# Kernel tuning notes

Measured on AMD Instinct MI355X. Metric: run time of the kernel, lower is better.

Reference implementation:

```python
import jax, jax.numpy as jnp
import numpy as np

E, D, H, K = 8, 768, 3072, 2   # num_experts, embed_size, expert_size, top-k
TAU = 1.0
BN, PN = 32, 196

def l2norm(v):
    # F.normalize(p=2, dim=-1), eps=1e-12
    return v / jnp.maximum(jnp.linalg.norm(v, axis=-1, keepdims=True), 1e-12)

def setup_inputs() -> dict:
    key = jax.random.key(0)
    ks = jax.random.split(key, 8)
    s = 0.02  # weight init scale for stability
    return {
        "x": jax.random.normal(ks[0], (BN, PN, D), dtype=jnp.float32),
        "Wlinear": jax.random.normal(ks[1], (D, D), dtype=jnp.float32) * s,
        "learnedE": jax.random.normal(ks[2], (E, D), dtype=jnp.float32),
        "bias": jnp.zeros((BN * PN, E), dtype=jnp.float32),
        "W1": jax.random.normal(ks[3], (E, D, H), dtype=jnp.float32) * s,
        "b1": jnp.zeros((E, H), dtype=jnp.float32),
        "W2": jax.random.normal(ks[4], (E, H, D), dtype=jnp.float32) * s,
        "b2": jnp.zeros((E, D), dtype=jnp.float32),
        "sW1": jax.random.normal(ks[5], (D, H), dtype=jnp.float32) * s,
        "sb1": jnp.zeros((H,), dtype=jnp.float32),
        "sW2": jax.random.normal(ks[6], (H, D), dtype=jnp.float32) * s,
        "sb2": jnp.zeros((D,), dtype=jnp.float32),
    }

def reference(x, Wlinear, learnedE, bias, W1, b1, W2, b2, sW1, sb1, sW2, sb2):
    bn, pn, d = x.shape
    patches = x.reshape(bn * pn, d)                      # [T, D]
    proj = l2norm(patches @ Wlinear.T)                   # router projection
    routed = proj @ l2norm(learnedE).T                   # [T, E] cosine scores
    probs = jax.nn.softmax((routed + bias) / TAU, axis=1)  # eval path (no noise)
    k_probs, k_idx = jax.lax.top_k(probs, K)             # [T, K]
    # combine weights: scatter top-k probs into dense [T, E] gate matrix
    T = probs.shape[0]
    gates = jnp.zeros_like(probs).at[jnp.arange(T)[:, None], k_idx].add(k_probs)
    # expert MLPs computed densely for all experts, masked by gates
    h = jax.nn.gelu(jnp.einsum('td,edh->teh', patches, W1) + b1[None], approximate=False)
    eo = jnp.einsum('teh,ehd->ted', h, W2) + b2[None]    # [T, E, D]
    moe = jnp.einsum('ted,te->td', eo, gates)            # weighted combine
    # shared expert (expert_list[-1]) applied to every token; dropout is identity in eval
    shared = jax.nn.gelu(patches @ sW1 + sb1, approximate=False) @ sW2 + sb2
    return (moe + shared).reshape(bn, pn, d)
```

## Files before the change

### kernel.cpp

```cpp
#include <hip/hip_runtime.h>
#include <hip/hip_bf16.h>

typedef __hip_bfloat16 bf16;
typedef __attribute__((ext_vector_type(8))) short short8;
typedef __attribute__((ext_vector_type(4))) float f32x4;

#define T_TOK 6272
#define D_DIM 768
#define H_DIM 3072
#define NEXP 8
#define MAXTILES 160

__device__ __forceinline__ void async16(void* lds, const void* g) {
  __builtin_amdgcn_global_load_lds(
      (const __attribute__((address_space(1))) void*)g,
      (__attribute__((address_space(3))) void*)lds, 16, 0, 0);
}


__global__ void cast_hilo(const float* __restrict__ in, bf16* __restrict__ hi,
                          bf16* __restrict__ lo, int n) {
  int i = blockIdx.x * blockDim.x + threadIdx.x;
  int stride = gridDim.x * blockDim.x;
  for (; i < n; i += stride) {
    float x = in[i];
    bf16 h = __float2bfloat16(x);
    hi[i] = h;
    lo[i] = __float2bfloat16(x - __bfloat162float(h));
  }
}

__global__ void transpose_cast(const float* __restrict__ in, bf16* __restrict__ out,
                               int R, int C) {
  __shared__ float tile[32][33];
  int b = blockIdx.z;
  const float* ib = in + (size_t)b * R * C;
  bf16* ob = out + (size_t)b * R * C;
  int r0 = blockIdx.x * 32, c0 = blockIdx.y * 32;
  int tx = threadIdx.x & 31, ty = threadIdx.x >> 5;
  for (int i = 0; i < 32; i += 8)
    tile[ty + i][tx] = ib[(size_t)(r0 + ty + i) * C + c0 + tx];
  __syncthreads();
  for (int i = 0; i < 32; i += 8)
    ob[(size_t)(c0 + ty + i) * R + r0 + tx] = __float2bfloat16(tile[tx][ty + i]);
}

__global__ void norm_learnedE(const float* __restrict__ lE, float* __restrict__ eHat) {
  int wave = threadIdx.x >> 6, lane = threadIdx.x & 63;
  for (int e = wave; e < NEXP; e += 4) {
    float v[12];
    float ss = 0.f;
    for (int j = 0; j < 12; j++) {
      v[j] = lE[e * D_DIM + lane + 64 * j];
      ss += v[j] * v[j];
    }
    for (int o = 32; o; o >>= 1) ss += __shfl_xor(ss, o);
    float rn = 1.f / fmaxf(sqrtf(ss), 1e-12f);
    for (int j = 0; j < 12; j++) eHat[e * D_DIM + lane + 64 * j] = v[j] * rn;
  }
}


__global__ __launch_bounds__(256) void gemm_router(
    const bf16* __restrict__ pHi, const bf16* __restrict__ pLo,
    const bf16* __restrict__ wHi, const bf16* __restrict__ wLo,
    float* __restrict__ y) {
  __shared__ __align__(16) bf16 As[128 * 32];
  __shared__ __align__(16) bf16 Bs[128 * 32];
  int tid = threadIdx.x, wave = tid >> 6, lane = tid & 63;
  int wr = wave >> 1, wc = wave & 1;
  int rowbase = blockIdx.x * 128, colbase = blockIdx.y * 128;
  int sc8 = (lane & 3) * 8;
  f32x4 acc[4][4];
  for (int m = 0; m < 4; m++)
    for (int n = 0; n < 4; n++) acc[m][n] = 0.f;

  for (int ks = 0; ks < 72; ks++) {
    int term = ks / 24;
    int kk = (ks % 24) * 32;
    const bf16* A = (term == 1) ? pLo : pHi;
    const bf16* B = (term == 2) ? wLo : wHi;
    __syncthreads();
    for (int p = 0; p < 2; p++) {
      int r = wave * 32 + p * 16 + (lane >> 2);
      async16(&As[(wave * 32 + p * 16) * 32], A + (size_t)(rowbase + r) * D_DIM + kk + sc8);
      async16(&Bs[(wave * 32 + p * 16) * 32], B + (size_t)(colbase + r) * D_DIM + kk + sc8);
    }
    __syncthreads();
    int koff = (lane >> 4) * 8;
    short8 af[4], bfr[4];
    for (int m = 0; m < 4; m++)
      af[m] = *(const short8*)&As[(wr * 64 + m * 16 + (lane & 15)) * 32 + koff];
    for (int n = 0; n < 4; n++)
      bfr[n] = *(const short8*)&Bs[(wc * 64 + n * 16 + (lane & 15)) * 32 + koff];
    for (int m = 0; m < 4; m++)
      for (int n = 0; n < 4; n++)
        acc[m][n] = __builtin_amdgcn_mfma_f32_16x16x32_bf16(af[m], bfr[n], acc[m][n], 0, 0, 0);
  }
  for (int m = 0; m < 4; m++)
    for (int n = 0; n < 4; n++)
      for (int j = 0; j < 4; j++) {
        int r = rowbase + wr * 64 + m * 16 + (lane >> 4) * 4 + j;
        int c = colbase + wc * 64 + n * 16 + (lane & 15);
        y[(size_t)r * D_DIM + c] = acc[m][n][j];
      }
}


__global__ void router_epi(const float* __restrict__ y, const float* __restrict__ eHat,
                           const float* __restrict__ bias, int* __restrict__ gidx,
                           float* __restrict__ gval, int* __restrict__ counts) {
  int wave = threadIdx.x >> 6, lane = threadIdx.x & 63;
  int t = blockIdx.x * 4 + wave;
  float v[12];
  float ss = 0.f;
  for (int j = 0; j < 12; j++) {
    v[j] = y[(size_t)t * D_DIM + lane + 64 * j];
    ss += v[j] * v[j];
  }
  for (int o = 32; o; o >>= 1) ss += __shfl_xor(ss, o);
  float d[NEXP];
  for (int e = 0; e < NEXP; e++) {
    float s = 0.f;
    for (int j = 0; j < 12; j++) s += v[j] * eHat[e * D_DIM + lane + 64 * j];
    for (int o = 32; o; o >>= 1) s += __shfl_xor(s, o);
    d[e] = s;
  }
  if (lane == 0) {
    float rn = 1.f / fmaxf(sqrtf(ss), 1e-12f);
    float sc[NEXP], mx = -1e30f;
    for (int e = 0; e < NEXP; e++) {
      sc[e] = d[e] * rn + bias[t * NEXP + e];
      mx = fmaxf(mx, sc[e]);
    }
    float p[NEXP], sum = 0.f;
    for (int e = 0; e < NEXP; e++) {
      p[e] = expf(sc[e] - mx);
      sum += p[e];
    }
    float inv = 1.f / sum;
    int i1 = 0;
    for (int e = 1; e < NEXP; e++)
      if (sc[e] > sc[i1]) i1 = e;
    int i2 = -1;
    for (int e = 0; e < NEXP; e++) {
      if (e == i1) continue;
      if (i2 < 0 || sc[e] > sc[i2]) i2 = e;
    }
    gidx[t * 2] = i1;
    gidx[t * 2 + 1] = i2;
    gval[t * 2] = p[i1] * inv;
    gval[t * 2 + 1] = p[i2] * inv;
    atomicAdd(&counts[i1], 1);
    atomicAdd(&counts[i2], 1);
  }
}


__global__ void scan_build(const int* __restrict__ counts, int* __restrict__ segstart,
                           int* __restrict__ cursors, int* __restrict__ tiles,
                           int* __restrict__ numtiles) {
  if (threadIdx.x == 0) {
    int off = 0;
    for (int e = 0; e < NEXP; e++) {
      segstart[e] = off;
      cursors[e] = off;
      off += counts[e];
    }
    segstart[NEXP] = off;
    segstart[NEXP + 1] = off + T_TOK;
    int nt = 0;
    for (int e = 0; e < NEXP + 1; e++) {
      int cnt = (e < NEXP) ? counts[e] : T_TOK;
      int ntl = (cnt + 127) >> 7;
      for (int l = 0; l < ntl; l++) {
        tiles[nt * 2] = e;
        tiles[nt * 2 + 1] = l;
        nt++;
      }
    }
    *numtiles = nt;
  }
}

__global__ void fill_assign(const int* __restrict__ gidx, int* __restrict__ cursors,
                            int* __restrict__ rowtok, int* __restrict__ slot_of) {
  int t = blockIdx.x * 256 + threadIdx.x;
  if (t >= T_TOK) return;
  for (int k = 0; k < 2; k++) {
    int e = gidx[t * 2 + k];
    int pos = atomicAdd(&cursors[e], 1);
    rowtok[pos] = t;
    slot_of[t * 2 + k] = pos;
  }
  rowtok[2 * T_TOK + t] = t;
}


__global__ __launch_bounds__(256) void gemm_ffn1(
    const bf16* __restrict__ pHi, const bf16* __restrict__ W1T,
    const bf16* __restrict__ sW1T, const float* __restrict__ b1,
    const float* __restrict__ sb1, const int* __restrict__ segstart,
    const int* __restrict__ tiles, const int* __restrict__ numtiles,
    const int* __restrict__ rowtok, bf16* __restrict__ hbuf) {
  int gx = blockIdx.x;
  if (gx >= *numtiles) return;
  int seg = tiles[gx * 2], lt = tiles[gx * 2 + 1];
  int s0 = segstart[seg] + lt * 128;
  int send = segstart[seg + 1];
  const bf16* Bw = (seg < NEXP) ? W1T + (size_t)seg * H_DIM * D_DIM : sW1T;
  const float* bb = (seg < NEXP) ? b1 + seg * H_DIM : sb1;

  __shared__ __align__(16) bf16 As[128 * 32];
  __shared__ __align__(16) bf16 Bs[128 * 32];
  int tid = threadIdx.x, wave = tid >> 6, lane = tid & 63;
  int wr = wave >> 1, wc = wave & 1;
  int colbase = blockIdx.y * 128;
  int sc8 = (lane & 3) * 8;

  const bf16* arow[2];
  for (int p = 0; p < 2; p++) {
    int s = s0 + wave * 32 + p * 16 + (lane >> 2);
    if (s > send - 1) s = send - 1;
    arow[p] = pHi + (size_t)rowtok[s] * D_DIM;
  }

  f32x4 acc[4][4];
  for (int m = 0; m < 4; m++)
    for (int n = 0; n < 4; n++) acc[m][n] = 0.f;

  for (int ks = 0; ks < 24; ks++) {
    int kk = ks * 32;
    __syncthreads();
    for (int p = 0; p < 2; p++) {
      int r = wave * 32 + p * 16 + (lane >> 2);
      async16(&As[(wave * 32 + p * 16) * 32], arow[p] + kk + sc8);
      async16(&Bs[(wave * 32 + p * 16) * 32], Bw + (size_t)(colbase + r) * D_DIM + kk + sc8);
    }
    __syncthreads();
    int koff = (lane >> 4) * 8;
    short8 af[4], bfr[4];
    for (int m = 0; m < 4; m++)
      af[m] = *(const short8*)&As[(wr * 64 + m * 16 + (lane & 15)) * 32 + koff];
    for (int n = 0; n < 4; n++)
      bfr[n] = *(const short8*)&Bs[(wc * 64 + n * 16 + (lane & 15)) * 32 + koff];
    for (int m = 0; m < 4; m++)
      for (int n = 0; n < 4; n++)
        acc[m][n] = __builtin_amdgcn_mfma_f32_16x16x32_bf16(af[m], bfr[n], acc[m][n], 0, 0, 0);
  }
  for (int n = 0; n < 4; n++) {
    int c = colbase + wc * 64 + n * 16 + (lane & 15);
    float bv = bb[c];
    for (int m = 0; m < 4; m++)
      for (int j = 0; j < 4; j++) {
        int s = s0 + wr * 64 + m * 16 + (lane >> 4) * 4 + j;
        if (s < send) {
          float xv = acc[m][n][j] + bv;
          float g = 0.5f * xv * (1.f + erff(xv * 0.70710678118654752f));
          hbuf[(size_t)s * H_DIM + c] = __float2bfloat16(g);
        }
      }
  }
}


__global__ __launch_bounds__(256) void gemm_ffn2(
    const bf16* __restrict__ hbuf, const bf16* __restrict__ W2T,
    const bf16* __restrict__ sW2T, const float* __restrict__ b2,
    const float* __restrict__ sb2, const int* __restrict__ segstart,
    const int* __restrict__ tiles, const int* __restrict__ numtiles,
    float* __restrict__ moebuf) {
  int gx = blockIdx.x;
  if (gx >= *numtiles) return;
  int seg = tiles[gx * 2], lt = tiles[gx * 2 + 1];
  int s0 = segstart[seg] + lt * 128;
  int send = segstart[seg + 1];
  const bf16* Bw = (seg < NEXP) ? W2T + (size_t)seg * H_DIM * D_DIM : sW2T;
  const float* bb = (seg < NEXP) ? b2 + seg * D_DIM : sb2;

  __shared__ __align__(16) bf16 As[128 * 32];
  __shared__ __align__(16) bf16 Bs[128 * 32];
  int tid = threadIdx.x, wave = tid >> 6, lane = tid & 63;
  int wr = wave >> 1, wc = wave & 1;
  int colbase = blockIdx.y * 128;
  int sc8 = (lane & 3) * 8;

  f32x4 acc[4][4];
  for (int m = 0; m < 4; m++)
    for (int n = 0; n < 4; n++) acc[m][n] = 0.f;

  for (int ks = 0; ks < 96; ks++) {
    int kk = ks * 32;
    __syncthreads();
    for (int p = 0; p < 2; p++) {
      int r = wave * 32 + p * 16 + (lane >> 2);
      async16(&As[(wave * 32 + p * 16) * 32], hbuf + (size_t)(s0 + r) * H_DIM + kk + sc8);
      async16(&Bs[(wave * 32 + p * 16) * 32], Bw + (size_t)(colbase + r) * H_DIM + kk + sc8);
    }
    __syncthreads();
    int koff = (lane >> 4) * 8;
    short8 af[4], bfr[4];
    for (int m = 0; m < 4; m++)
      af[m] = *(const short8*)&As[(wr * 64 + m * 16 + (lane & 15)) * 32 + koff];
    for (int n = 0; n < 4; n++)
      bfr[n] = *(const short8*)&Bs[(wc * 64 + n * 16 + (lane & 15)) * 32 + koff];
    for (int m = 0; m < 4; m++)
      for (int n = 0; n < 4; n++)
        acc[m][n] = __builtin_amdgcn_mfma_f32_16x16x32_bf16(af[m], bfr[n], acc[m][n], 0, 0, 0);
  }
  for (int n = 0; n < 4; n++) {
    int c = colbase + wc * 64 + n * 16 + (lane & 15);
    float bv = bb[c];
    for (int m = 0; m < 4; m++)
      for (int j = 0; j < 4; j++) {
        int s = s0 + wr * 64 + m * 16 + (lane >> 4) * 4 + j;
        if (s < send) moebuf[(size_t)s * D_DIM + c] = acc[m][n][j] + bv;
      }
  }
}


__global__ void combine_out(const float* __restrict__ moebuf, const float* __restrict__ gval,
                            const int* __restrict__ slot_of, float* __restrict__ out) {
  int i = blockIdx.x * 256 + threadIdx.x;
  const int total = T_TOK * (D_DIM / 4);
  if (i >= total) return;
  int t = i / (D_DIM / 4), c = i % (D_DIM / 4);
  float g0 = gval[2 * t], g1 = gval[2 * t + 1];
  int sA = slot_of[2 * t], sB = slot_of[2 * t + 1];
  const f32x4* pa = (const f32x4*)(moebuf + (size_t)sA * D_DIM) + c;
  const f32x4* pb = (const f32x4*)(moebuf + (size_t)sB * D_DIM) + c;
  const f32x4* ps = (const f32x4*)(moebuf + (size_t)(2 * T_TOK + t) * D_DIM) + c;
  f32x4 r = g0 * (*pa) + g1 * (*pb) + *ps;
  ((f32x4*)out)[i] = r;
}


extern "C" void kernel_launch(void* const* d_in, const int* in_sizes, int n_in,
                              void* d_out, int out_size, void* d_ws, size_t ws_size,
                              hipStream_t stream) {
  const float* x = (const float*)d_in[0];
  const float* Wlinear = (const float*)d_in[1];
  const float* learnedE = (const float*)d_in[2];
  const float* bias = (const float*)d_in[3];
  const float* W1 = (const float*)d_in[4];
  const float* b1 = (const float*)d_in[5];
  const float* W2 = (const float*)d_in[6];
  const float* b2 = (const float*)d_in[7];
  const float* sW1 = (const float*)d_in[8];
  const float* sb1 = (const float*)d_in[9];
  const float* sW2 = (const float*)d_in[10];
  const float* sb2 = (const float*)d_in[11];
  float* out = (float*)d_out;

  char* ws = (char*)d_ws;
  size_t off = 0;
  auto alloc = [&](size_t bytes) {
    char* p = ws + off;
    off += (bytes + 255) & ~(size_t)255;
    return p;
  };
  float* eHat = (float*)alloc(8 * 768 * 4);
  bf16* pHi = (bf16*)alloc((size_t)T_TOK * D_DIM * 2);
  bf16* pLo = (bf16*)alloc((size_t)T_TOK * D_DIM * 2);
  bf16* wHi = (bf16*)alloc((size_t)D_DIM * D_DIM * 2);
  bf16* wLo = (bf16*)alloc((size_t)D_DIM * D_DIM * 2);
  bf16* W1T = (bf16*)alloc((size_t)NEXP * D_DIM * H_DIM * 2);
  bf16* W2T = (bf16*)alloc((size_t)NEXP * D_DIM * H_DIM * 2);
  bf16* sW1T = (bf16*)alloc((size_t)D_DIM * H_DIM * 2);
  bf16* sW2T = (bf16*)alloc((size_t)D_DIM * H_DIM * 2);
  float* y = (float*)alloc((size_t)T_TOK * D_DIM * 4);
  bf16* hbuf = (bf16*)alloc((size_t)3 * T_TOK * H_DIM * 2);
  float* moebuf = (float*)alloc((size_t)3 * T_TOK * D_DIM * 4);
  int* gidx = (int*)alloc(T_TOK * 2 * 4);
  float* gval = (float*)alloc(T_TOK * 2 * 4);
  int* rowtok = (int*)alloc(3 * T_TOK * 4);
  int* slot_of = (int*)alloc(T_TOK * 2 * 4);
  int* counts = (int*)alloc(8 * 4);
  int* segstart = (int*)alloc(10 * 4);
  int* cursors = (int*)alloc(8 * 4);
  int* numtiles = (int*)alloc(4);
  int* tiles = (int*)alloc(MAXTILES * 2 * 4);
  (void)ws_size; (void)in_sizes; (void)n_in; (void)out_size;

  hipMemsetAsync(counts, 0, 8 * 4, stream);
  norm_learnedE<<<1, 256, 0, stream>>>(learnedE, eHat);
  cast_hilo<<<2048, 256, 0, stream>>>(x, pHi, pLo, T_TOK * D_DIM);
  cast_hilo<<<1024, 256, 0, stream>>>(Wlinear, wHi, wLo, D_DIM * D_DIM);
  transpose_cast<<<dim3(D_DIM / 32, H_DIM / 32, NEXP), 256, 0, stream>>>(W1, W1T, D_DIM, H_DIM);
  transpose_cast<<<dim3(H_DIM / 32, D_DIM / 32, NEXP), 256, 0, stream>>>(W2, W2T, H_DIM, D_DIM);
  transpose_cast<<<dim3(D_DIM / 32, H_DIM / 32, 1), 256, 0, stream>>>(sW1, sW1T, D_DIM, H_DIM);
  transpose_cast<<<dim3(H_DIM / 32, D_DIM / 32, 1), 256, 0, stream>>>(sW2, sW2T, H_DIM, D_DIM);

  gemm_router<<<dim3(T_TOK / 128, D_DIM / 128), 256, 0, stream>>>(pHi, pLo, wHi, wLo, y);
  router_epi<<<T_TOK / 4, 256, 0, stream>>>(y, eHat, bias, gidx, gval, counts);
  scan_build<<<1, 64, 0, stream>>>(counts, segstart, cursors, tiles, numtiles);
  fill_assign<<<(T_TOK + 255) / 256, 256, 0, stream>>>(gidx, cursors, rowtok, slot_of);

  gemm_ffn1<<<dim3(MAXTILES, H_DIM / 128), 256, 0, stream>>>(
      pHi, W1T, sW1T, b1, sb1, segstart, tiles, numtiles, rowtok, hbuf);
  gemm_ffn2<<<dim3(MAXTILES, D_DIM / 128), 256, 0, stream>>>(
      hbuf, W2T, sW2T, b2, sb2, segstart, tiles, numtiles, moebuf);

  combine_out<<<(T_TOK * (D_DIM / 4) + 255) / 256, 256, 0, stream>>>(moebuf, gval, slot_of, out);
}
```

Measured before the change: 757.5 us.

## Enlarge grouped FFN GEMM tiles to 256x256 with 512 threads and cheaper GELU

The expert FFN GEMMs move from 128x128 tiles with 4 waves to 256x256 tiles with 8 waves. Each wave now holds 8x4 MFMA accumulators, and the tile builder and grid sizes are changed to match. The larger tiles are meant to raise data reuse per LDS load and cut redundant global traffic for the weights. The exact erff GELU is replaced by an Abramowitz-Stegun polynomial with __expf, which lowers epilogue cost but adds small approximation error. The trade-offs are higher register pressure, more padding waste in small expert segments, and fewer blocks in ffn2 (3 column tiles).

```diff
diff --git a/kernel.cpp b/kernel.cpp
--- a/kernel.cpp
+++ b/kernel.cpp
@@ -9,12 +9,24 @@
 #define D_DIM 768
 #define H_DIM 3072
 #define NEXP 8
-#define MAXTILES 160
+#define MAXTILES 96
 
 __device__ __forceinline__ void async16(void* lds, const void* g) {
   __builtin_amdgcn_global_load_lds(
       (const __attribute__((address_space(1))) void*)g,
       (__attribute__((address_space(3))) void*)lds, 16, 0, 0);
+}
+
+__device__ __forceinline__ float gelu_f(float x) {
+  float z = x * 0.70710678118654752f;
+  float az = fabsf(z);
+  float t = 1.f / (1.f + 0.3275911f * az);
+  float poly = ((((1.061405429f * t - 1.453152027f) * t + 1.421413741f) * t -
+                 0.284496736f) * t + 0.254829592f) * t;
+  float e = __expf(-az * az);
+  float er = 1.f - poly * e;
+  er = copysignf(er, z);
+  return 0.5f * x * (1.f + er);
 }
 
 
@@ -172,7 +184,7 @@
     int nt = 0;
     for (int e = 0; e < NEXP + 1; e++) {
       int cnt = (e < NEXP) ? counts[e] : T_TOK;
-      int ntl = (cnt + 127) >> 7;
+      int ntl = (cnt + 255) >> 8;
       for (int l = 0; l < ntl; l++) {
         tiles[nt * 2] = e;
         tiles[nt * 2 + 1] = l;
@@ -197,7 +209,7 @@
 }
 
 
-__global__ __launch_bounds__(256) void gemm_ffn1(
+__global__ __launch_bounds__(512) void gemm_ffn1(
     const bf16* __restrict__ pHi, const bf16* __restrict__ W1T,
     const bf16* __restrict__ sW1T, const float* __restrict__ b1,
     const float* __restrict__ sb1, const int* __restrict__ segstart,
@@ -206,65 +218,66 @@
   int gx = blockIdx.x;
   if (gx >= *numtiles) return;
   int seg = tiles[gx * 2], lt = tiles[gx * 2 + 1];
-  int s0 = segstart[seg] + lt * 128;
+  int s0 = segstart[seg] + lt * 256;
   int send = segstart[seg + 1];
   const bf16* Bw = (seg < NEXP) ? W1T + (size_t)seg * H_DIM * D_DIM : sW1T;
   const float* bb = (seg < NEXP) ? b1 + seg * H_DIM : sb1;
 
-  __shared__ __align__(16) bf16 As[128 * 32];
-  __shared__ __align__(16) bf16 Bs[128 * 32];
+  __shared__ __align__(16) bf16 As[256 * 32];
+  __shared__ __align__(16) bf16 Bs[256 * 32];
   int tid = threadIdx.x, wave = tid >> 6, lane = tid & 63;
-  int wr = wave >> 1, wc = wave & 1;
-  int colbase = blockIdx.y * 128;
+  int wr = wave >> 2, wc = wave & 3;
+  int colbase = blockIdx.y * 256;
   int sc8 = (lane & 3) * 8;
 
   const bf16* arow[2];
+  const bf16* brow[2];
   for (int p = 0; p < 2; p++) {
-    int s = s0 + wave * 32 + p * 16 + (lane >> 2);
+    int r = wave * 32 + p * 16 + (lane >> 2);
+    int s = s0 + r;
     if (s > send - 1) s = send - 1;
     arow[p] = pHi + (size_t)rowtok[s] * D_DIM;
-  }
-
-  f32x4 acc[4][4];
-  for (int m = 0; m < 4; m++)
+    brow[p] = Bw + (size_t)(colbase + r) * D_DIM;
+  }
+
+  f32x4 acc[8][4];
+  for (int m = 0; m < 8; m++)
     for (int n = 0; n < 4; n++) acc[m][n] = 0.f;
 
   for (int ks = 0; ks < 24; ks++) {
     int kk = ks * 32;
     __syncthreads();
     for (int p = 0; p < 2; p++) {
-      int r = wave * 32 + p * 16 + (lane >> 2);
       async16(&As[(wave * 32 + p * 16) * 32], arow[p] + kk + sc8);
-      async16(&Bs[(wave * 32 + p * 16) * 32], Bw + (size_t)(colbase + r) * D_DIM + kk + sc8);
+      async16(&Bs[(wave * 32 + p * 16) * 32], brow[p] + kk + sc8);
     }
     __syncthreads();
     int koff = (lane >> 4) * 8;
-    short8 af[4], bfr[4];
-    for (int m = 0; m < 4; m++)
-      af[m] = *(const short8*)&As[(wr * 64 + m * 16 + (lane & 15)) * 32 + koff];
+    short8 af[8], bfr[4];
+    for (int m = 0; m < 8; m++)
+      af[m] = *(const short8*)&As[(wr * 128 + m * 16 + (lane & 15)) * 32 + koff];
     for (int n = 0; n < 4; n++)
       bfr[n] = *(const short8*)&Bs[(wc * 64 + n * 16 + (lane & 15)) * 32 + koff];
-    for (int m = 0; m < 4; m++)
+    for (int m = 0; m < 8; m++)
       for (int n = 0; n < 4; n++)
         acc[m][n] = __builtin_amdgcn_mfma_f32_16x16x32_bf16(af[m], bfr[n], acc[m][n], 0, 0, 0);
   }
   for (int n = 0; n < 4; n++) {
     int c = colbase + wc * 64 + n * 16 + (lane & 15);
     float bv = bb[c];
-    for (int m = 0; m < 4; m++)
+    for (int m = 0; m < 8; m++)
       for (int j = 0; j < 4; j++) {
-        int s = s0 + wr * 64 + m * 16 + (lane >> 4) * 4 + j;
+        int s = s0 + wr * 128 + m * 16 + (lane >> 4) * 4 + j;
         if (s < send) {
           float xv = acc[m][n][j] + bv;
-          float g = 0.5f * xv * (1.f + erff(xv * 0.70710678118654752f));
-          hbuf[(size_t)s * H_DIM + c] = __float2bfloat16(g);
+          hbuf[(size_t)s * H_DIM + c] = __float2bfloat16(gelu_f(xv));
         }
       }
   }
 }
 
 
-__global__ __launch_bounds__(256) void gemm_ffn2(
+__global__ __launch_bounds__(512) void gemm_ffn2(
     const bf16* __restrict__ hbuf, const bf16* __restrict__ W2T,
     const bf16* __restrict__ sW2T, const float* __restrict__ b2,
     const float* __restrict__ sb2, const int* __restrict__ segstart,
@@ -273,47 +286,56 @@
   int gx = blockIdx.x;
   if (gx >= *numtiles) return;
   int seg = tiles[gx * 2], lt = tiles[gx * 2 + 1];
-  int s0 = segstart[seg] + lt * 128;
+  int s0 = segstart[seg] + lt * 256;
   int send = segstart[seg + 1];
   const bf16* Bw = (seg < NEXP) ? W2T + (size_t)seg * H_DIM * D_DIM : sW2T;
   const float* bb = (seg < NEXP) ? b2 + seg * D_DIM : sb2;
 
-  __shared__ __align__(16) bf16 As[128 * 32];
-  __shared__ __align__(16) bf16 Bs[128 * 32];
+  __shared__ __align__(16) bf16 As[256 * 32];
+  __shared__ __align__(16) bf16 Bs[256 * 32];
   int tid = threadIdx.x, wave = tid >> 6, lane = tid & 63;
-  int wr = wave >> 1, wc = wave & 1;
-  int colbase = blockIdx.y * 128;
+  int wr = wave >> 2, wc = wave & 3;
+  int colbase = blockIdx.y * 256;
   int sc8 = (lane & 3) * 8;
 
-  f32x4 acc[4][4];
-  for (int m = 0; m < 4; m++)
+  const bf16* arow[2];
+  const bf16* brow[2];
+  for (int p = 0; p < 2; p++) {
+    int r = wave * 32 + p * 16 + (lane >> 2);
+    int s = s0 + r;
+    if (s > send - 1) s = send - 1;
+    arow[p] = hbuf + (size_t)s * H_DIM;
+    brow[p] = Bw + (size_t)(colbase + r) * H_DIM;
+  }
+
+  f32x4 acc[8][4];
+  for (int m = 0; m < 8; m++)
     for (int n = 0; n < 4; n++) acc[m][n] = 0.f;
 
   for (int ks = 0; ks < 96; ks++) {
     int kk = ks * 32;
     __syncthreads();
     for (int p = 0; p < 2; p++) {
-      int r = wave * 32 + p * 16 + (lane >> 2);
-      async16(&As[(wave * 32 + p * 16) * 32], hbuf + (size_t)(s0 + r) * H_DIM + kk + sc8);
-      async16(&Bs[(wave * 32 + p * 16) * 32], Bw + (size_t)(colbase + r) * H_DIM + kk + sc8);
+      async16(&As[(wave * 32 + p * 16) * 32], arow[p] + kk + sc8);
+      async16(&Bs[(wave * 32 + p * 16) * 32], brow[p] + kk + sc8);
     }
     __syncthreads();
     int koff = (lane >> 4) * 8;
-    short8 af[4], bfr[4];
-    for (int m = 0; m < 4; m++)
-      af[m] = *(const short8*)&As[(wr * 64 + m * 16 + (lane & 15)) * 32 + koff];
+    short8 af[8], bfr[4];
+    for (int m = 0; m < 8; m++)
+      af[m] = *(const short8*)&As[(wr * 128 + m * 16 + (lane & 15)) * 32 + koff];
     for (int n = 0; n < 4; n++)
       bfr[n] = *(const short8*)&Bs[(wc * 64 + n * 16 + (lane & 15)) * 32 + koff];
-    for (int m = 0; m < 4; m++)
+    for (int m = 0; m < 8; m++)
       for (int n = 0; n < 4; n++)
         acc[m][n] = __builtin_amdgcn_mfma_f32_16x16x32_bf16(af[m], bfr[n], acc[m][n], 0, 0, 0);
   }
   for (int n = 0; n < 4; n++) {
     int c = colbase + wc * 64 + n * 16 + (lane & 15);
     float bv = bb[c];
-    for (int m = 0; m < 4; m++)
+    for (int m = 0; m < 8; m++)
       for (int j = 0; j < 4; j++) {
-        int s = s0 + wr * 64 + m * 16 + (lane >> 4) * 4 + j;
+        int s = s0 + wr * 128 + m * 16 + (lane >> 4) * 4 + j;
         if (s < send) moebuf[(size_t)s * D_DIM + c] = acc[m][n][j] + bv;
       }
   }
@@ -397,9 +419,9 @@
   scan_build<<<1, 64, 0, stream>>>(counts, segstart, cursors, tiles, numtiles);
   fill_assign<<<(T_TOK + 255) / 256, 256, 0, stream>>>(gidx, cursors, rowtok, slot_of);
 
-  gemm_ffn1<<<dim3(MAXTILES, H_DIM / 128), 256, 0, stream>>>(
+  gemm_ffn1<<<dim3(MAXTILES, H_DIM / 256), 512, 0, stream>>>(
       pHi, W1T, sW1T, b1, sb1, segstart, tiles, numtiles, rowtok, hbuf);
-  gemm_ffn2<<<dim3(MAXTILES, D_DIM / 128), 256, 0, stream>>>(
+  gemm_ffn2<<<dim3(MAXTILES, D_DIM / 256), 512, 0, stream>>>(
       hbuf, W2T, sW2T, b2, sb2, segstart, tiles, numtiles, moebuf);
 
   combine_out<<<(T_TOK * (D_DIM / 4) + 255) / 256, 256, 0, stream>>>(moebuf, gval, slot_of, out);
```

Result: slower. 2.100 ms (+177.3%).

## Double-buffer LDS tiles in router and FFN GEMMs, use polynomial erf GELU

Applied to the files above, without the earlier changes.

Converts the three GEMM kernels from single-buffered LDS with two barriers per k-step to double-buffered tiles, issuing the async global-to-LDS loads for the next k-step before running the MFMAs on the current one. This is meant to overlap memory latency with matrix math and drop one barrier per step. The exact erff GELU is replaced with an Abramowitz-Stegun polynomial approximation using __expf to cut epilogue cost. The GELU change adds small approximation error (about 1e-7 in erf). The single barrier per step relies on the async loads being complete by the time it is reached, since there is no explicit wait on the LDS DMA.

```diff
diff --git a/kernel.cpp b/kernel.cpp
--- a/kernel.cpp
+++ b/kernel.cpp
@@ -15,6 +15,18 @@
   __builtin_amdgcn_global_load_lds(
       (const __attribute__((address_space(1))) void*)g,
       (__attribute__((address_space(3))) void*)lds, 16, 0, 0);
+}
+
+__device__ __forceinline__ float gelu_f(float x) {
+  float z = x * 0.70710678118654752f;
+  float az = fabsf(z);
+  float t = 1.f / (1.f + 0.3275911f * az);
+  float poly = ((((1.061405429f * t - 1.453152027f) * t + 1.421413741f) * t -
+                 0.284496736f) * t + 0.254829592f) * t;
+  float e = __expf(-az * az);
+  float er = 1.f - poly * e;
+  er = copysignf(er, z);
+  return 0.5f * x * (1.f + er);
 }
 
 
@@ -65,37 +77,60 @@
     const bf16* __restrict__ pHi, const bf16* __restrict__ pLo,
     const bf16* __restrict__ wHi, const bf16* __restrict__ wLo,
     float* __restrict__ y) {
-  __shared__ __align__(16) bf16 As[128 * 32];
-  __shared__ __align__(16) bf16 Bs[128 * 32];
+  __shared__ __align__(16) bf16 As[2][128 * 32];
+  __shared__ __align__(16) bf16 Bs[2][128 * 32];
   int tid = threadIdx.x, wave = tid >> 6, lane = tid & 63;
   int wr = wave >> 1, wc = wave & 1;
   int rowbase = blockIdx.x * 128, colbase = blockIdx.y * 128;
   int sc8 = (lane & 3) * 8;
-  f32x4 acc[4][4];
-  for (int m = 0; m < 4; m++)
-    for (int n = 0; n < 4; n++) acc[m][n] = 0.f;
-
-  for (int ks = 0; ks < 72; ks++) {
+
+  size_t aoff[2], boff[2];
+  for (int p = 0; p < 2; p++) {
+    int r = wave * 32 + p * 16 + (lane >> 2);
+    aoff[p] = (size_t)(rowbase + r) * D_DIM + sc8;
+    boff[p] = (size_t)(colbase + r) * D_DIM + sc8;
+  }
+
+  auto stage = [&](int buf, int ks) {
     int term = ks / 24;
-    int kk = (ks % 24) * 32;
     const bf16* A = (term == 1) ? pLo : pHi;
     const bf16* B = (term == 2) ? wLo : wHi;
-    __syncthreads();
+    int kk = (ks - term * 24) * 32;
+#pragma unroll
     for (int p = 0; p < 2; p++) {
-      int r = wave * 32 + p * 16 + (lane >> 2);
-      async16(&As[(wave * 32 + p * 16) * 32], A + (size_t)(rowbase + r) * D_DIM + kk + sc8);
-      async16(&Bs[(wave * 32 + p * 16) * 32], B + (size_t)(colbase + r) * D_DIM + kk + sc8);
-    }
-    __syncthreads();
+      async16(&As[buf][(wave * 32 + p * 16) * 32], A + aoff[p] + kk);
+      async16(&Bs[buf][(wave * 32 + p * 16) * 32], B + boff[p] + kk);
+    }
+  };
+
+  f32x4 acc[4][4];
+#pragma unroll
+  for (int m = 0; m < 4; m++)
+#pragma unroll
+    for (int n = 0; n < 4; n++) acc[m][n] = 0.f;
+
+  stage(0, 0);
+  __syncthreads();
+  int cur = 0;
+  for (int ks = 0; ks < 72; ks++) {
+    if (ks < 71) stage(cur ^ 1, ks + 1);
     int koff = (lane >> 4) * 8;
+    const bf16* Ac = As[cur];
+    const bf16* Bc = Bs[cur];
     short8 af[4], bfr[4];
-    for (int m = 0; m < 4; m++)
-      af[m] = *(const short8*)&As[(wr * 64 + m * 16 + (lane & 15)) * 32 + koff];
+#pragma unroll
+    for (int m = 0; m < 4; m++)
+      af[m] = *(const short8*)&Ac[(wr * 64 + m * 16 + (lane & 15)) * 32 + koff];
+#pragma unroll
     for (int n = 0; n < 4; n++)
-      bfr[n] = *(const short8*)&Bs[(wc * 64 + n * 16 + (lane & 15)) * 32 + koff];
-    for (int m = 0; m < 4; m++)
+      bfr[n] = *(const short8*)&Bc[(wc * 64 + n * 16 + (lane & 15)) * 32 + koff];
+#pragma unroll
+    for (int m = 0; m < 4; m++)
+#pragma unroll
       for (int n = 0; n < 4; n++)
         acc[m][n] = __builtin_amdgcn_mfma_f32_16x16x32_bf16(af[m], bfr[n], acc[m][n], 0, 0, 0);
+    __syncthreads();
+    cur ^= 1;
   }
   for (int m = 0; m < 4; m++)
     for (int n = 0; n < 4; n++)
@@ -211,53 +246,73 @@
   const bf16* Bw = (seg < NEXP) ? W1T + (size_t)seg * H_DIM * D_DIM : sW1T;
   const float* bb = (seg < NEXP) ? b1 + seg * H_DIM : sb1;
 
-  __shared__ __align__(16) bf16 As[128 * 32];
-  __shared__ __align__(16) bf16 Bs[128 * 32];
+  __shared__ __align__(16) bf16 As[2][128 * 32];
+  __shared__ __align__(16) bf16 Bs[2][128 * 32];
   int tid = threadIdx.x, wave = tid >> 6, lane = tid & 63;
   int wr = wave >> 1, wc = wave & 1;
   int colbase = blockIdx.y * 128;
   int sc8 = (lane & 3) * 8;
 
   const bf16* arow[2];
+  const bf16* brow[2];
   for (int p = 0; p < 2; p++) {
-    int s = s0 + wave * 32 + p * 16 + (lane >> 2);
+    int r = wave * 32 + p * 16 + (lane >> 2);
+    int s = s0 + r;
     if (s > send - 1) s = send - 1;
-    arow[p] = pHi + (size_t)rowtok[s] * D_DIM;
-  }
+    arow[p] = pHi + (size_t)rowtok[s] * D_DIM + sc8;
+    brow[p] = Bw + (size_t)(colbase + r) * D_DIM + sc8;
+  }
+
+  auto stage = [&](int buf, int ks) {
+    int kk = ks * 32;
+#pragma unroll
+    for (int p = 0; p < 2; p++) {
+      async16(&As[buf][(wave * 32 + p * 16) * 32], arow[p] + kk);
+      async16(&Bs[buf][(wave * 32 + p * 16) * 32], brow[p] + kk);
+    }
+  };
 
   f32x4 acc[4][4];
+#pragma unroll
   for (int m = 0; m < 4; m++)
+#pragma unroll
     for (int n = 0; n < 4; n++) acc[m][n] = 0.f;
 
+  stage(0, 0);
+  __syncthreads();
+  int cur = 0;
   for (int ks = 0; ks < 24; ks++) {
-    int kk = ks * 32;
-    __syncthreads();
-    for (int p = 0; p < 2; p++) {
-      int r = wave * 32 + p * 16 + (lane >> 2);
-      async16(&As[(wave * 32 + p * 16) * 32], arow[p] + kk + sc8);
-      async16(&Bs[(wave * 32 + p * 16) * 32], Bw + (size_t)(colbase + r) * D_DIM + kk + sc8);
-    }
-    __syncthreads();
+    if (ks < 23) stage(cur ^ 1, ks + 1);
     int koff = (lane >> 4) * 8;
+    const bf16* Ac = As[cur];
+    const bf16* Bc = Bs[cur];
     short8 af[4], bfr[4];
-    for (int m = 0; m < 4; m++)
-      af[m] = *(const short8*)&As[(wr * 64 + m * 16 + (lane & 15)) * 32 + koff];
+#pragma unroll
+    for (int m = 0; m < 4; m++)
+      af[m] = *(const short8*)&Ac[(wr * 64 + m * 16 + (lane & 15)) * 32 + koff];
+#pragma unroll
     for (int n = 0; n < 4; n++)
-      bfr[n] = *(const short8*)&Bs[(wc * 64 + n * 16 + (lane & 15)) * 32 + koff];
-    for (int m = 0; m < 4; m++)
+      bfr[n] = *(const short8*)&Bc[(wc * 64 + n * 16 + (lane & 15)) * 32 + koff];
+#pragma unroll
+    for (int m = 0; m < 4; m++)
+#pragma unroll
       for (int n = 0; n < 4; n++)
         acc[m][n] = __builtin_amdgcn_mfma_f32_16x16x32_bf16(af[m], bfr[n], acc[m][n], 0, 0, 0);
-  }
+    __syncthreads();
+    cur ^= 1;
+  }
+#pragma unroll
   for (int n = 0; n < 4; n++) {
     int c = colbase + wc * 64 + n * 16 + (lane & 15);
     float bv = bb[c];
-    for (int m = 0; m < 4; m++)
+#pragma unroll
+    for (int m = 0; m < 4; m++)
+#pragma unroll
       for (int j = 0; j < 4; j++) {
         int s = s0 + wr * 64 + m * 16 + (lane >> 4) * 4 + j;
         if (s < send) {
           float xv = acc[m][n][j] + bv;
-          float g = 0.5f * xv * (1.f + erff(xv * 0.70710678118654752f));
-          hbuf[(size_t)s * H_DIM + c] = __float2bfloat16(g);
+          hbuf[(size_t)s * H_DIM + c] = __float2bfloat16(gelu_f(xv));
         }
       }
   }
@@ -278,40 +333,68 @@
   const bf16* Bw = (seg < NEXP) ? W2T + (size_t)seg * H_DIM * D_DIM : sW2T;
   const float* bb = (seg < NEXP) ? b2 + seg * D_DIM : sb2;
 
-  __shared__ __align__(16) bf16 As[128 * 32];
-  __shared__ __align__(16) bf16 Bs[128 * 32];
+  __shared__ __align__(16) bf16 As[2][128 * 32];
+  __shared__ __align__(16) bf16 Bs[2][128 * 32];
   int tid = threadIdx.x, wave = tid >> 6, lane = tid & 63;
   int wr = wave >> 1, wc = wave & 1;
   int colbase = blockIdx.y * 128;
   int sc8 = (lane & 3) * 8;
 
+  const bf16* arow[2];
+  const bf16* brow[2];
+  for (int p = 0; p < 2; p++) {
+    int r = wave * 32 + p * 16 + (lane >> 2);
+    int s = s0 + r;
+    if (s > send - 1) s = send - 1;
+    arow[p] = hbuf + (size_t)s * H_DIM + sc8;
+    brow[p] = Bw + (size_t)(colbase + r) * H_DIM + sc8;
+  }
+
+  auto stage = [&](int buf, int ks) {
+    int kk = ks * 32;
+#pragma unroll
+    for (int p = 0; p < 2; p++) {
+      async16(&As[buf][(wave * 32 + p * 16) * 32], arow[p] + kk);
+      async16(&Bs[buf][(wave * 32 + p * 16) * 32], brow[p] + kk);
+    }
+  };
+
   f32x4 acc[4][4];
+#pragma unroll
   for (int m = 0; m < 4; m++)
+#pragma unroll
     for (int n = 0; n < 4; n++) acc[m][n] = 0.f;
 
+  stage(0, 0);
+  __syncthreads();
+  int cur = 0;
   for (int ks = 0; ks < 96; ks++) {
-    int kk = ks * 32;
-    __syncthreads();
-    for (int p = 0; p < 2; p++) {
-      int r = wave * 32 + p * 16 + (lane >> 2);
-      async16(&As[(wave * 32 + p * 16) * 32], hbuf + (size_t)(s0 + r) * H_DIM + kk + sc8);
-      async16(&Bs[(wave * 32 + p * 16) * 32], Bw + (size_t)(colbase + r) * H_DIM + kk + sc8);
-    }
-    __syncthreads();
+    if (ks < 95) stage(cur ^ 1, ks + 1);
     int koff = (lane >> 4) * 8;
+    const bf16* Ac = As[cur];
+    const bf16* Bc = Bs[cur];
     short8 af[4], bfr[4];
-    for (int m = 0; m < 4; m++)
-      af[m] = *(const short8*)&As[(wr * 64 + m * 16 + (lane & 15)) * 32 + koff];
+#pragma unroll
+    for (int m = 0; m < 4; m++)
+      af[m] = *(const short8*)&Ac[(wr * 64 + m * 16 + (lane & 15)) * 32 + koff];
+#pragma unroll
     for (int n = 0; n < 4; n++)
-      bfr[n] = *(const short8*)&Bs[(wc * 64 + n * 16 + (lane & 15)) * 32 + koff];
-    for (int m = 0; m < 4; m++)
+      bfr[n] = *(const short8*)&Bc[(wc * 64 + n * 16 + (lane & 15)) * 32 + koff];
+#pragma unroll
+    for (int m = 0; m < 4; m++)
+#pragma unroll
       for (int n = 0; n < 4; n++)
         acc[m][n] = __builtin_amdgcn_mfma_f32_16x16x32_bf16(af[m], bfr[n], acc[m][n], 0, 0, 0);
-  }
+    __syncthreads();
+    cur ^= 1;
+  }
+#pragma unroll
   for (int n = 0; n < 4; n++) {
     int c = colbase + wc * 64 + n * 16 + (lane & 15);
     float bv = bb[c];
-    for (int m = 0; m < 4; m++)
+#pragma unroll
+    for (int m = 0; m < 4; m++)
+#pragma unroll
       for (int j = 0; j < 4; j++) {
         int s = s0 + wr * 64 + m * 16 + (lane >> 4) * 4 + j;
         if (s < send) moebuf[(size_t)s * D_DIM + c] = acc[m][n][j] + bv;
```

Measured after the change: 797.0 us. 5.2% more time.
